# Performance work log

Measured on AMD Instinct MI355X. Metric: run time of the kernel, lower is better.

The kernel has to match this reference:

```python
import jax, jax.numpy as jnp
import numpy as np

NEG_INF = -1e30
EPS = 1e-7  # keras.backend.epsilon()


def _ctc_loss(y_true, y_pred):
    """Faithful CTC loss matching keras ctc_batch_cost + tf v1 ctc_loss.

    y_true: [B, L] int labels (no blanks), all rows full length L.
    y_pred: [B, T, C] probabilities; tf ctc_loss re-softmaxes log(p+eps).
    Blank index = C - 1. Returns loss [B, 1].
    """
    B, T, C = y_pred.shape
    L = y_true.shape[1]
    S = 2 * L + 1
    blank = C - 1

    # keras passes log(y_pred+eps) as logits; tf ctc_loss applies softmax
    lp = jax.nn.log_softmax(jnp.log(y_pred + EPS), axis=-1)  # [B,T,C]

    # extended label sequence: blank, l0, blank, l1, ..., blank  [B,S]
    ext = jnp.full((B, S), blank, dtype=y_true.dtype)
    ext = ext.at[:, 1::2].set(y_true)

    # skip transition (s-2 -> s) allowed iff ext[s] != blank and ext[s] != ext[s-2]
    same_as_2back = jnp.concatenate(
        [jnp.ones((B, 2), bool), ext[:, 2:] == ext[:, :-2]], axis=1)
    can_skip = (ext != blank) & (~same_as_2back)  # [B,S]

    # emission log-prob of each lattice state at each time: [B,T,S]
    lp_ext = jnp.take_along_axis(lp, ext[:, None, :], axis=2)

    # alpha init at t=0: only states 0 (blank) and 1 (first label) reachable
    alpha0 = jnp.full((B, S), NEG_INF, dtype=lp.dtype)
    alpha0 = alpha0.at[:, 0].set(lp_ext[:, 0, 0])
    alpha0 = alpha0.at[:, 1].set(lp_ext[:, 0, 1])

    pad1 = jnp.full((B, 1), NEG_INF, dtype=lp.dtype)
    pad2 = jnp.full((B, 2), NEG_INF, dtype=lp.dtype)

    def step(alpha, lp_t):
        a_stay = alpha
        a_prev = jnp.concatenate([pad1, alpha[:, :-1]], axis=1)
        a_skip = jnp.where(can_skip,
                           jnp.concatenate([pad2, alpha[:, :-2]], axis=1),
                           NEG_INF)
        m = jnp.maximum(a_stay, jnp.maximum(a_prev, a_skip))
        lse = m + jnp.log(jnp.exp(a_stay - m) + jnp.exp(a_prev - m)
                          + jnp.exp(a_skip - m))
        return lse + lp_t, None

    # scan over remaining T-1 time steps
    alphaT, _ = jax.lax.scan(step, alpha0, jnp.swapaxes(lp_ext, 0, 1)[1:])

    # total log-likelihood: end at last blank or last label
    loglik = jnp.logaddexp(alphaT[:, S - 1], alphaT[:, S - 2])
    return -loglik[:, None]  # [B,1], matches expand_dims(..., 1)


def setup_inputs() -> dict:
    key = jax.random.key(0)
    k1, k2 = jax.random.split(key)
    B, T, C, L = 128, 1024, 128, 128
    y_true = jax.random.randint(k1, (B, L), 0, C - 1, dtype=jnp.int32)
    y_pred = jax.random.uniform(k2, (B, T, C), dtype=jnp.float32)
    return {"y_true": y_true, "y_pred": y_pred}


def reference(y_true, y_pred):
    return _ctc_loss(y_true, y_pred)
```

## Files before the change

kernel.cpp:

```cpp
#include <hip/hip_runtime.h>

#define TT 1024
#define CC 128
#define LL 128
#define EPSF 1e-7f
#define LN2F 0.69314718055994531f

#define LOG2F(x) __builtin_amdgcn_logf(x)

typedef unsigned int uint;
typedef uint uintx4 __attribute__((ext_vector_type(4)));

template <int CTRL>
__device__ __forceinline__ int dpp_i(int old_, int x) {
  return __builtin_amdgcn_update_dpp(old_, x, CTRL, 0xf, 0xf, false);
}
__device__ __forceinline__ float dpp_shr1_f32(float x) {
  return __uint_as_float((uint)__builtin_amdgcn_update_dpp(
      0, (int)__float_as_uint(x), 0x138, 0xf, 0xf, true));
}

__device__ __forceinline__ uint bf16bits(float x) {
  uint u = __float_as_uint(x);
  return (u + 0x7fffu + ((u >> 16) & 1u)) >> 16;
}

#define GL16(gp, lp)                                            \
  __builtin_amdgcn_global_load_lds(                             \
      (const __attribute__((address_space(1))) void*)(gp),      \
      (__attribute__((address_space(3))) void*)(lp), 16, 0, 0)
#define GL4(gp, lp)                                             \
  __builtin_amdgcn_global_load_lds(                             \
      (const __attribute__((address_space(1))) void*)(gp),      \
      (__attribute__((address_space(3))) void*)(lp), 4, 0, 0)

__global__ __launch_bounds__(512) void prep_kernel(const int* __restrict__ yt,
                                                   const float* __restrict__ yp,
                                                   uint* __restrict__ ET,
                                                   float* __restrict__ EB) {
  const int tid = threadIdx.x;
  const int w = tid >> 6;
  const int L = tid & 63;
  const int b = blockIdx.x >> 7;
  const int tg = blockIdx.x & 127;
  const int t = tg * 8 + w;

  __shared__ float rowp[8][130];
  __shared__ uint tp[64][9];

  const float* P = yp + ((size_t)b * TT + t) * CC;
  const float2 v = *(const float2*)(P + 2 * L);
  float x = (v.x + EPSF) + (v.y + EPSF);
#pragma unroll
  for (int off = 32; off > 0; off >>= 1) x += __shfl_xor(x, off);
  const float r = 1.0f / x;
  const float er = EPSF * r;
  *(float2*)&rowp[w][2 * L] =
      make_float2(__builtin_fmaf(v.x, r, er), __builtin_fmaf(v.y, r, er));
  const int2 lab = *(const int2*)(yt + b * LL + 2 * L);
  if (L == 63) EB[b * TT + t] = __builtin_fmaf(v.y, r, er);
  __syncthreads();
  const float p1 = rowp[w][lab.x];
  const float p2 = rowp[w][lab.y];
  tp[L][w] = (bf16bits(p2) << 16) | bf16bits(p1);
  __syncthreads();
  if (tid < 128) {
    const int g4 = tid >> 6, Lo = tid & 63;
    uint4 val;
    val.x = tp[Lo][g4 * 4 + 0];
    val.y = tp[Lo][g4 * 4 + 1];
    val.z = tp[Lo][g4 * 4 + 2];
    val.w = tp[Lo][g4 * 4 + 3];
    ((uint4*)ET)[((size_t)(b * 256 + tg * 2 + g4) << 6) + Lo] = val;
  }
}


#define CTC_STEP(wv, pbf)                                   \
  do {                                                      \
    const float p1 = __uint_as_float((wv) << 16);           \
    const float p2 = __uint_as_float((wv) & 0xffff0000u);   \
    const float pb = (pbf);                                 \
    const float p3 = dpp_shr1_f32(a3);                      \
    const float n0 = (a0 + p3) * pb;                        \
    const float n1 = __builtin_fmaf(s1f, p3, a0 + a1) * p1; \
    const float n2 = (a2 + a1) * pb;                        \
    const float n3 = __builtin_fmaf(s3f, a1, a3 + a2) * p2; \
    const float n4 = (a4 + a3) * pb;                        \
    a0 = n0; a1 = n1; a2 = n2; a3 = n3; a4 = n4;            \
  } while (0)

#define CTC_QUAD(et, eb)      \
  do {                        \
    CTC_STEP((et).x, (eb).x); \
    CTC_STEP((et).y, (eb).y); \
    CTC_STEP((et).z, (eb).z); \
    CTC_STEP((et).w, (eb).w); \
  } while (0)

#define CTC_RESCALE()                                                \
  do {                                                               \
    const float m = fmaxf(fmaxf(fmaxf(a0, a1), fmaxf(a2, a3)), a4);  \
    int ke = (int)(__float_as_uint(m) >> 23);                        \
    ke = max(ke, dpp_i<0x111>(ke, ke));                              \
    ke = max(ke, dpp_i<0x112>(ke, ke));                              \
    ke = max(ke, dpp_i<0x114>(ke, ke));                              \
    ke = max(ke, dpp_i<0x118>(ke, ke));                              \
    ke = max(ke, dpp_i<0x142>(ke, ke));                              \
    ke = max(ke, dpp_i<0x143>(ke, ke));                              \
    ke = __builtin_amdgcn_readlane(ke, 63);                          \
    int e = ke - 227;             \
    e = e < -127 ? -127 : e;                                         \
    const float sc = __uint_as_float((uint)(127 - e) << 23);         \
    a0 *= sc; a1 *= sc; a2 *= sc; a3 *= sc; a4 *= sc;                \
    ell += e;                                                        \
  } while (0)

__global__ __launch_bounds__(128) void scan_kernel(const int* __restrict__ yt,
                                                   const uint* __restrict__ ET,
                                                   const float* __restrict__ EB,
                                                   float* __restrict__ out) {
  const int b = blockIdx.x;
  const int tid = threadIdx.x;
  const int L = tid & 63;
  const int wv = tid >> 6;

  __shared__ uint4 ETl[4][8][64];
  __shared__ float4 EBl[256];

  const int2 lab = *(const int2*)(yt + b * LL + 2 * L);
  const int labm1 = __shfl_up(lab.y, 1);
  const float s1f = ((L > 0) && (lab.x != labm1)) ? 1.0f : 0.0f;
  const float s3f = (lab.y != lab.x) ? 1.0f : 0.0f;

  const uintx4* Et = (const uintx4*)ET + ((size_t)b << 14) + L;
  const float* Bp = EB + b * TT;

  if (wv == 1) {
#pragma unroll
    for (int k = 0; k < 16; ++k) GL4(Bp + k * 64 + L, (char*)EBl + k * 256);
#pragma unroll
    for (int g = 0; g < 16; ++g) GL16(Et + g * 64, (char*)ETl + g * 1024);
    asm volatile("s_waitcnt vmcnt(8)" ::: "memory");
  }
  __syncthreads();

  uint4 etA, etB;
  float4 ebA, ebB;
  if (wv == 0) {
    etA = ((const uint4*)ETl)[L];
    ebA = EBl[0];
  }

  float a0 = (wv == 0 && L == 0) ? 0x1.0p100f : 0.0f;
  float a1 = 0.0f, a2 = 0.0f, a3 = 0.0f, a4 = 0.0f;
  int ell = -100;

#pragma unroll 1
  for (int kk = 0; kk < 32; ++kk) {
    if (wv == 1) {
      const int bb = (kk + 2 < 32) ? kk + 2 : 31;
      const uintx4* src = Et + (size_t)bb * 512;
      char* dst = (char*)ETl + (size_t)((kk + 2) & 3) * 8192;
#pragma unroll
      for (int g = 0; g < 8; ++g) GL16(src + g * 64, dst + g * 1024);
      asm volatile("s_waitcnt vmcnt(8)" ::: "memory");
    } else {
      const uint4* cur = (const uint4*)ETl + (size_t)(kk & 3) * 512;
      const int ebi = kk * 8;
      etB = cur[1 * 64 + L]; ebB = EBl[ebi + 1];
      CTC_QUAD(etA, ebA);
      etA = cur[2 * 64 + L]; ebA = EBl[ebi + 2];
      CTC_QUAD(etB, ebB);
      etB = cur[3 * 64 + L]; ebB = EBl[ebi + 3];
      CTC_QUAD(etA, ebA);
      etA = cur[4 * 64 + L]; ebA = EBl[ebi + 4];
      CTC_QUAD(etB, ebB);
      CTC_RESCALE();
      etB = cur[5 * 64 + L]; ebB = EBl[ebi + 5];
      CTC_QUAD(etA, ebA);
      etA = cur[6 * 64 + L]; ebA = EBl[ebi + 6];
      CTC_QUAD(etB, ebB);
      etB = cur[7 * 64 + L]; ebB = EBl[ebi + 7];
      CTC_QUAD(etA, ebA);
      etA = ((const uint4*)ETl)[(size_t)((kk + 1) & 3) * 512 + L];
      ebA = EBl[(ebi + 8 < 256) ? ebi + 8 : 255];
      CTC_QUAD(etB, ebB);
      CTC_RESCALE();
    }
    __syncthreads();
  }

  if (tid == 63) {
    float s = a3 + a4;
    if (s < 1e-37f) s = 1e-37f;
    out[b] = -LN2F * ((float)ell + LOG2F(s));
  }
}

extern "C" void kernel_launch(void* const* d_in, const int* in_sizes, int n_in,
                              void* d_out, int out_size, void* d_ws,
                              size_t ws_size, hipStream_t stream) {
  const int* yt = (const int*)d_in[0];
  const float* yp = (const float*)d_in[1];
  float* out = (float*)d_out;
  const int B = in_sizes[0] / LL;
  uint* ET = (uint*)d_ws;
  float* EB = (float*)((char*)d_ws + (size_t)B * 64 * TT * 4);
  hipLaunchKernelGGL(prep_kernel, dim3(B * 128), dim3(512), 0, stream, yt, yp,
                     ET, EB);
  hipLaunchKernelGGL(scan_kernel, dim3(B), dim3(128), 0, stream, yt, ET, EB,
                     out);
}
```

Before: 152.4 us.

## Fuse emission prep into scan kernel with producer warps computing in-block

Drops the separate prep kernel and its workspace round trip. In one fused kernel, four producer wavefronts read the raw probabilities, normalise each row, gather label probabilities with ds_bpermute, pack them to bf16 and write them into an LDS ring that the scan wavefront consumes. This removes one launch and the global write and re-read of the emission tensor. In exchange, each block of 128 now handles the full probability read and the softmax work itself, with only 128 blocks on the device, so the producers must keep pace with the serial scan.

```diff
diff --git a/kernel.cpp b/kernel.cpp
--- a/kernel.cpp
+++ b/kernel.cpp
@@ -9,7 +9,6 @@
 #define LOG2F(x) __builtin_amdgcn_logf(x)
 
 typedef unsigned int uint;
-typedef uint uintx4 __attribute__((ext_vector_type(4)));
 
 template <int CTRL>
 __device__ __forceinline__ int dpp_i(int old_, int x) {
@@ -25,54 +24,9 @@
   return (u + 0x7fffu + ((u >> 16) & 1u)) >> 16;
 }
 
-#define GL16(gp, lp)                                            \
-  __builtin_amdgcn_global_load_lds(                             \
-      (const __attribute__((address_space(1))) void*)(gp),      \
-      (__attribute__((address_space(3))) void*)(lp), 16, 0, 0)
-#define GL4(gp, lp)                                             \
-  __builtin_amdgcn_global_load_lds(                             \
-      (const __attribute__((address_space(1))) void*)(gp),      \
-      (__attribute__((address_space(3))) void*)(lp), 4, 0, 0)
-
-__global__ __launch_bounds__(512) void prep_kernel(const int* __restrict__ yt,
-                                                   const float* __restrict__ yp,
-                                                   uint* __restrict__ ET,
-                                                   float* __restrict__ EB) {
-  const int tid = threadIdx.x;
-  const int w = tid >> 6;
-  const int L = tid & 63;
-  const int b = blockIdx.x >> 7;
-  const int tg = blockIdx.x & 127;
-  const int t = tg * 8 + w;
-
-  __shared__ float rowp[8][130];
-  __shared__ uint tp[64][9];
-
-  const float* P = yp + ((size_t)b * TT + t) * CC;
-  const float2 v = *(const float2*)(P + 2 * L);
-  float x = (v.x + EPSF) + (v.y + EPSF);
-#pragma unroll
-  for (int off = 32; off > 0; off >>= 1) x += __shfl_xor(x, off);
-  const float r = 1.0f / x;
-  const float er = EPSF * r;
-  *(float2*)&rowp[w][2 * L] =
-      make_float2(__builtin_fmaf(v.x, r, er), __builtin_fmaf(v.y, r, er));
-  const int2 lab = *(const int2*)(yt + b * LL + 2 * L);
-  if (L == 63) EB[b * TT + t] = __builtin_fmaf(v.y, r, er);
-  __syncthreads();
-  const float p1 = rowp[w][lab.x];
-  const float p2 = rowp[w][lab.y];
-  tp[L][w] = (bf16bits(p2) << 16) | bf16bits(p1);
-  __syncthreads();
-  if (tid < 128) {
-    const int g4 = tid >> 6, Lo = tid & 63;
-    uint4 val;
-    val.x = tp[Lo][g4 * 4 + 0];
-    val.y = tp[Lo][g4 * 4 + 1];
-    val.z = tp[Lo][g4 * 4 + 2];
-    val.w = tp[Lo][g4 * 4 + 3];
-    ((uint4*)ET)[((size_t)(b * 256 + tg * 2 + g4) << 6) + Lo] = val;
-  }
+__device__ __forceinline__ float bperm(int byteaddr, float v) {
+  return __uint_as_float(
+      (uint)__builtin_amdgcn_ds_bpermute(byteaddr, (int)__float_as_uint(v)));
 }
 
 
@@ -116,77 +70,107 @@
     ell += e;                                                        \
   } while (0)
 
-__global__ __launch_bounds__(128) void scan_kernel(const int* __restrict__ yt,
-                                                   const uint* __restrict__ ET,
-                                                   const float* __restrict__ EB,
-                                                   float* __restrict__ out) {
+#define STAGE8(t0)                                                          \
+  do {                                                                      \
+    float2 vv[8];                                                           \
+    _Pragma("unroll") for (int j = 0; j < 8; ++j)                           \
+        vv[j] = *(const float2*)(Pb + (size_t)((t0) + j) * CC);             \
+    _Pragma("unroll") for (int q = 0; q < 2; ++q) {                         \
+      uint wds[4];                                                          \
+      float nys[4];                                                         \
+      _Pragma("unroll") for (int c = 0; c < 4; ++c) {                       \
+        const int j = q * 4 + c;                                            \
+        float x = (vv[j].x + EPSF) + (vv[j].y + EPSF);                      \
+        _Pragma("unroll") for (int off = 32; off > 0; off >>= 1)            \
+            x += __shfl_xor(x, off);                                        \
+        const float r = 1.0f / x;                                           \
+        const float er = EPSF * r;                                          \
+        const float nx = __builtin_fmaf(vv[j].x, r, er);                    \
+        const float ny = __builtin_fmaf(vv[j].y, r, er);                    \
+        const float c1a = bperm(gxb, nx), c1b = bperm(gxb, ny);             \
+        const float c2a = bperm(gyb, nx), c2b = bperm(gyb, ny);             \
+        const float g1 = sx ? c1b : c1a;                                    \
+        const float g2 = sy ? c2b : c2a;                                    \
+        wds[c] = (bf16bits(g2) << 16) | bf16bits(g1);                       \
+        nys[c] = ny;                                                        \
+      }                                                                     \
+      const int tq = (t0) + q * 4;                                          \
+      uint4 val;                                                            \
+      val.x = wds[0]; val.y = wds[1]; val.z = wds[2]; val.w = wds[3];       \
+      *(uint4*)((char*)ETl + ((tq >> 5) & 3) * 8192 +                       \
+                ((tq >> 2) & 7) * 1024 + L * 16) = val;                     \
+      if (L == 63) {                                                        \
+        float4 e4;                                                          \
+        e4.x = nys[0]; e4.y = nys[1]; e4.z = nys[2]; e4.w = nys[3];         \
+        *(float4*)&EBl[tq] = e4;                                            \
+      }                                                                     \
+    }                                                                       \
+  } while (0)
+
+__global__ __launch_bounds__(320) void ctc_fused(const int* __restrict__ yt,
+                                                 const float* __restrict__ yp,
+                                                 float* __restrict__ out) {
   const int b = blockIdx.x;
   const int tid = threadIdx.x;
   const int L = tid & 63;
-  const int wv = tid >> 6;
+  const int w = tid >> 6;
 
   __shared__ uint4 ETl[4][8][64];
-  __shared__ float4 EBl[256];
+  __shared__ __align__(16) float EBl[TT];
 
   const int2 lab = *(const int2*)(yt + b * LL + 2 * L);
+
   const int labm1 = __shfl_up(lab.y, 1);
   const float s1f = ((L > 0) && (lab.x != labm1)) ? 1.0f : 0.0f;
   const float s3f = (lab.y != lab.x) ? 1.0f : 0.0f;
 
-  const uintx4* Et = (const uintx4*)ET + ((size_t)b << 14) + L;
-  const float* Bp = EB + b * TT;
+  const float* Pb = yp + (size_t)b * TT * CC + 2 * L;
+  const int gxb = (lab.x >> 1) << 2, gyb = (lab.y >> 1) << 2;
+  const int sx = lab.x & 1, sy = lab.y & 1;
 
-  if (wv == 1) {
-#pragma unroll
-    for (int k = 0; k < 16; ++k) GL4(Bp + k * 64 + L, (char*)EBl + k * 256);
-#pragma unroll
-    for (int g = 0; g < 16; ++g) GL16(Et + g * 64, (char*)ETl + g * 1024);
-    asm volatile("s_waitcnt vmcnt(8)" ::: "memory");
+  if (w != 0) {
+    STAGE8((w - 1) * 8);
+    STAGE8(32 + (w - 1) * 8);
   }
   __syncthreads();
 
-  uint4 etA, etB;
-  float4 ebA, ebB;
-  if (wv == 0) {
+  uint4 etA = {0, 0, 0, 0}, etB = {0, 0, 0, 0};
+  float4 ebA = {0, 0, 0, 0}, ebB = {0, 0, 0, 0};
+  if (w == 0) {
     etA = ((const uint4*)ETl)[L];
-    ebA = EBl[0];
+    ebA = *(const float4*)&EBl[0];
   }
 
-  float a0 = (wv == 0 && L == 0) ? 0x1.0p100f : 0.0f;
+  float a0 = (w == 0 && L == 0) ? 0x1.0p100f : 0.0f;
   float a1 = 0.0f, a2 = 0.0f, a3 = 0.0f, a4 = 0.0f;
   int ell = -100;
 
 #pragma unroll 1
   for (int kk = 0; kk < 32; ++kk) {
-    if (wv == 1) {
-      const int bb = (kk + 2 < 32) ? kk + 2 : 31;
-      const uintx4* src = Et + (size_t)bb * 512;
-      char* dst = (char*)ETl + (size_t)((kk + 2) & 3) * 8192;
-#pragma unroll
-      for (int g = 0; g < 8; ++g) GL16(src + g * 64, dst + g * 1024);
-      asm volatile("s_waitcnt vmcnt(8)" ::: "memory");
-    } else {
+    if (w == 0) {
       const uint4* cur = (const uint4*)ETl + (size_t)(kk & 3) * 512;
-      const int ebi = kk * 8;
-      etB = cur[1 * 64 + L]; ebB = EBl[ebi + 1];
+      const float4* ebp = (const float4*)&EBl[kk * 32];
+      etB = cur[1 * 64 + L]; ebB = ebp[1];
       CTC_QUAD(etA, ebA);
-      etA = cur[2 * 64 + L]; ebA = EBl[ebi + 2];
+      etA = cur[2 * 64 + L]; ebA = ebp[2];
       CTC_QUAD(etB, ebB);
-      etB = cur[3 * 64 + L]; ebB = EBl[ebi + 3];
+      etB = cur[3 * 64 + L]; ebB = ebp[3];
       CTC_QUAD(etA, ebA);
-      etA = cur[4 * 64 + L]; ebA = EBl[ebi + 4];
+      etA = cur[4 * 64 + L]; ebA = ebp[4];
       CTC_QUAD(etB, ebB);
       CTC_RESCALE();
-      etB = cur[5 * 64 + L]; ebB = EBl[ebi + 5];
+      etB = cur[5 * 64 + L]; ebB = ebp[5];
       CTC_QUAD(etA, ebA);
-      etA = cur[6 * 64 + L]; ebA = EBl[ebi + 6];
+      etA = cur[6 * 64 + L]; ebA = ebp[6];
       CTC_QUAD(etB, ebB);
-      etB = cur[7 * 64 + L]; ebB = EBl[ebi + 7];
+      etB = cur[7 * 64 + L]; ebB = ebp[7];
       CTC_QUAD(etA, ebA);
       etA = ((const uint4*)ETl)[(size_t)((kk + 1) & 3) * 512 + L];
-      ebA = EBl[(ebi + 8 < 256) ? ebi + 8 : 255];
+      ebA = *(const float4*)&EBl[(kk < 31) ? (kk + 1) * 32 : 1020];
       CTC_QUAD(etB, ebB);
       CTC_RESCALE();
+    } else if (kk < 30) {
+      STAGE8((kk + 2) * 32 + (w - 1) * 8);
     }
     __syncthreads();
   }
@@ -201,14 +185,10 @@
 extern "C" void kernel_launch(void* const* d_in, const int* in_sizes, int n_in,
                               void* d_out, int out_size, void* d_ws,
                               size_t ws_size, hipStream_t stream) {
+  (void)d_ws; (void)ws_size; (void)n_in; (void)out_size;
   const int* yt = (const int*)d_in[0];
   const float* yp = (const float*)d_in[1];
   float* out = (float*)d_out;
   const int B = in_sizes[0] / LL;
-  uint* ET = (uint*)d_ws;
-  float* EB = (float*)((char*)d_ws + (size_t)B * 64 * TT * 4);
-  hipLaunchKernelGGL(prep_kernel, dim3(B * 128), dim3(512), 0, stream, yt, yp,
-                     ET, EB);
-  hipLaunchKernelGGL(scan_kernel, dim3(B), dim3(128), 0, stream, yt, ET, EB,
-                     out);
+  hipLaunchKernelGGL(ctc_fused, dim3(B), dim3(320), 0, stream, yt, yp, out);
 }
```

After: 155.6 us. 1.02x slower.
